# Performance work log

Hardware: AMD Instinct MI355X
Metric: run time of the kernel (lower is better)

## Reference

```python
import jax, jax.numpy as jnp
import numpy as np

BITW = 1
BITA = 3
BATCH = 8192
IN_CH = 4096
N_UNITS = 4096


def _quantize(x, k):
    # DoReFa uniform quantizer with straight-through estimator (round -> identity grad)
    n = float(2 ** k - 1)
    return x + jax.lax.stop_gradient(jnp.round(x * n) / n - x)


def _cabs(x):
    # clip magnitude to [0, 1]
    return jnp.minimum(1.0, jnp.abs(x))


def quantize_active(x, bitA):
    if bitA == 32:
        return x
    return _quantize(x, bitA)


def quantize_weight(w, bitW):
    if bitW == 32:
        return w
    if bitW == 1:
        # binary weights scaled by mean |w| (E is treated as constant)
        E = jax.lax.stop_gradient(jnp.mean(jnp.abs(w)))
        y = w / E
        # sign with straight-through gradient
        return (y + jax.lax.stop_gradient(jnp.sign(y) - y)) * E
    t = jnp.tanh(w)
    t = t / jnp.max(jnp.abs(t)) * 0.5 + 0.5
    return 2.0 * _quantize(t, bitW) - 1.0


def setup_inputs() -> dict:
    key = jax.random.key(0)
    k1, k2 = jax.random.split(key)
    inputs = jax.random.normal(k1, (BATCH, IN_CH), dtype=jnp.float32)
    # truncated_normal(stddev=0.1) init approximated with normal * 0.1
    W = jax.random.normal(k2, (IN_CH, N_UNITS), dtype=jnp.float32) * 0.1
    b = jnp.zeros((N_UNITS,), dtype=jnp.float32)
    return {"inputs": inputs, "W": W, "b": b}


def reference(inputs, W, b):
    q_in = quantize_active(_cabs(inputs), BITA)   # [B, IN] in {0..1} grid of 2^bitA-1 levels
    q_W = quantize_weight(W, BITW)                # [IN, OUT] binary (+-E)
    out = jnp.matmul(q_in, q_W) + b               # [B, OUT]
    return out
```

## Files before the change

kernel.cpp:

```cpp
#include <hip/hip_runtime.h>


static constexpr int BATCH  = 8192;
static constexpr int IN_CH  = 4096;
static constexpr int NUNITS = 4096;
static constexpr int TPB    = 256;

typedef int v4i __attribute__((ext_vector_type(4)));

static constexpr size_t A8_OFF   = 0;
static constexpr size_t A8_BYTES = (size_t)BATCH * IN_CH;
static constexpr size_t BT_OFF   = A8_OFF + A8_BYTES;
static constexpr size_t BT_BYTES = (size_t)NUNITS * IN_CH;
static constexpr int    NPART    = 4096;
static constexpr size_t PART_OFF = BT_OFF + BT_BYTES;
static constexpr size_t SCALE_OFF= PART_OFF + NPART * sizeof(float);

__global__ __launch_bounds__(TPB) void k_scale(const float* __restrict__ partials,
                                               float* __restrict__ scale) {
    __shared__ float red[TPB];
    float s = 0.f;
    for (int i = threadIdx.x; i < NPART; i += TPB) s += partials[i];
    red[threadIdx.x] = s;
    __syncthreads();
    for (int off = TPB / 2; off > 0; off >>= 1) {
        if ((int)threadIdx.x < off) red[threadIdx.x] += red[threadIdx.x + off];
        __syncthreads();
    }
    if (threadIdx.x == 0) {
        float E = red[0] / (float)((size_t)IN_CH * NUNITS);
        *scale = E / 7.0f;
    }
}

__device__ __forceinline__ unsigned int q4(float4 v) {
    unsigned int b0 = (unsigned int)(int)rintf(fminf(1.0f, fabsf(v.x)) * 7.0f);
    unsigned int b1 = (unsigned int)(int)rintf(fminf(1.0f, fabsf(v.y)) * 7.0f);
    unsigned int b2 = (unsigned int)(int)rintf(fminf(1.0f, fabsf(v.z)) * 7.0f);
    unsigned int b3 = (unsigned int)(int)rintf(fminf(1.0f, fabsf(v.w)) * 7.0f);
    return b0 | (b1 << 8) | (b2 << 16) | (b3 << 24);
}

__global__ __launch_bounds__(TPB) void k_quant_a(const float4* __restrict__ x4,
                                                 uint4* __restrict__ a16) {
    const size_t t = (size_t)blockIdx.x * TPB + threadIdx.x;
    uint4 o;
    o.x = q4(x4[t * 4 + 0]);
    o.y = q4(x4[t * 4 + 1]);
    o.z = q4(x4[t * 4 + 2]);
    o.w = q4(x4[t * 4 + 3]);
    a16[t] = o;
}

__global__ __launch_bounds__(TPB) void k_signT(const float* __restrict__ W,
                                               char* __restrict__ bt,
                                               float* __restrict__ partials) {
    __shared__ char tile[64][68];
    __shared__ float red[TPB];
    const int bk = blockIdx.x & 63;
    const int bn = blockIdx.x >> 6;
    const int t  = threadIdx.x;
    const int c  = t & 63;
    const int r0 = t >> 6;
    float asum = 0.f;
#pragma unroll
    for (int i = 0; i < 16; ++i) {
        int r = i * 4 + r0;
        float w = W[(size_t)(bk * 64 + r) * NUNITS + bn * 64 + c];
        asum += fabsf(w);
        tile[c][r] = (w > 0.f) ? 1 : ((w < 0.f) ? -1 : 0);
    }
    __syncthreads();
    const int n  = t >> 2;
    const int kk = (t & 3) * 16;
    char o[16];
#pragma unroll
    for (int j = 0; j < 16; ++j) o[j] = tile[n][kk + j];
    *(uint4*)(bt + (size_t)(bn * 64 + n) * IN_CH + bk * 64 + kk) = *(const uint4*)o;

    red[t] = asum;
    __syncthreads();
    for (int off = TPB / 2; off > 0; off >>= 1) {
        if (t < off) red[t] += red[t + off];
        __syncthreads();
    }
    if (t == 0) partials[blockIdx.x] = red[0];
}

__device__ __forceinline__ void gload_lds16(const void* g, void* l) {
    __builtin_amdgcn_global_load_lds((const __attribute__((address_space(1))) void*)g,
                                     (__attribute__((address_space(3))) void*)l,
                                     16, 0, 0);
}

#define VMCNT4   asm volatile("s_waitcnt vmcnt(4)" ::: "memory")
#define VMCNT0   asm volatile("s_waitcnt vmcnt(0)" ::: "memory")
#define LGKM0    asm volatile("s_waitcnt lgkmcnt(0)" ::: "memory")
#define BARRIER  __builtin_amdgcn_s_barrier()
#define PRIO1    __builtin_amdgcn_s_setprio(1)
#define PRIO0    __builtin_amdgcn_s_setprio(0)

static constexpr int NT = IN_CH / 128;

__global__ __launch_bounds__(512, 2) void k_gemm(const char* __restrict__ A8,
                                                 const char* __restrict__ BT,
                                                 const float* __restrict__ scale_p,
                                                 const float* __restrict__ bias,
                                                 float* __restrict__ out) {
    __shared__ char As[2][32768];
    __shared__ char Bs[2][32768];

    const int t    = threadIdx.x;
    const int bid  = blockIdx.x;
    const int swzb = (bid & 7) * 64 + (bid >> 3);
    const int bRow = swzb >> 4;
    const int bCol = swzb & 15;
    const int lane = t & 63;
    const int wid  = t >> 6;
    const int wm   = wid >> 2;
    const int wn   = wid & 3;
    const int lr   = lane & 15;
    const int lk4  = lane >> 4;

    const size_t aBase = (size_t)(bRow * 256) * IN_CH;
    const size_t bBase = (size_t)(bCol * 256) * IN_CH;

    const int ceff0 = (lk4 * 16) ^ ((lr & 7) << 4);
    const int ceff1 = ceff0 ^ 64;

    const int srow  = t >> 3;
    const int scol  = ((t & 7) * 16) ^ ((srow & 7) << 4);
    const int sldso = t * 16;

    v4i acc[8][4] = {};
    v4i a0[4][2], a1[4][2], b01[2][2], b23[2][2];

#define STAGE(kt, q)                                                                  \
    do {                                                                              \
        const int _b = (kt) & 1;                                                      \
        if ((q) < 4)                                                                  \
            gload_lds16(A8 + aBase + (size_t)((q) * 64 + srow) * IN_CH + (kt) * 128 + scol, \
                        &As[_b][(q & 3) * 8192 + sldso]);                             \
        else                                                                          \
            gload_lds16(BT + bBase + (size_t)(((q) - 4) * 64 + srow) * IN_CH + (kt) * 128 + scol, \
                        &Bs[_b][((q) - 4) * 8192 + sldso]);                           \
    } while (0)

#define READ_A0(Ab)                                                    \
    _Pragma("unroll") for (int m = 0; m < 4; ++m) {                    \
        const int ra = (wm * 128 + m * 16 + lr) * 128;                 \
        a0[m][0] = *(const v4i*)((Ab) + ra + ceff0);                   \
        a0[m][1] = *(const v4i*)((Ab) + ra + ceff1);                   \
    }
#define READ_A1(Ab)                                                    \
    _Pragma("unroll") for (int m = 0; m < 4; ++m) {                    \
        const int ra = (wm * 128 + (m + 4) * 16 + lr) * 128;           \
        a1[m][0] = *(const v4i*)((Ab) + ra + ceff0);                   \
        a1[m][1] = *(const v4i*)((Ab) + ra + ceff1);                   \
    }
#define READ_B01(Bb)                                                   \
    _Pragma("unroll") for (int n = 0; n < 2; ++n) {                    \
        const int rb = (wn * 64 + n * 16 + lr) * 128;                  \
        b01[n][0] = *(const v4i*)((Bb) + rb + ceff0);                  \
        b01[n][1] = *(const v4i*)((Bb) + rb + ceff1);                  \
    }
#define READ_B23(Bb)                                                   \
    _Pragma("unroll") for (int n = 0; n < 2; ++n) {                    \
        const int rb = (wn * 64 + (n + 2) * 16 + lr) * 128;            \
        b23[n][0] = *(const v4i*)((Bb) + rb + ceff0);                  \
        b23[n][1] = *(const v4i*)((Bb) + rb + ceff1);                  \
    }
#define MFMA16(arr, brr, mo, no)                                                       \
    PRIO1;                                                                             \
    _Pragma("unroll") for (int m = 0; m < 4; ++m)                                      \
        _Pragma("unroll") for (int n = 0; n < 2; ++n)                                  \
            _Pragma("unroll") for (int s = 0; s < 2; ++s)                              \
                acc[(mo) + m][(no) + n] = __builtin_amdgcn_mfma_i32_16x16x64_i8(       \
                    arr[m][s], brr[n][s], acc[(mo) + m][(no) + n], 0, 0, 0);           \
    PRIO0

#pragma unroll
    for (int q = 0; q < 8; ++q) STAGE(0, q);
    STAGE(1, 0); STAGE(1, 1); STAGE(1, 2); STAGE(1, 3);
    VMCNT4;
    BARRIER;

    for (int T = 0; T < NT; ++T) {
        const char* Ab = As[T & 1];
        const char* Bb = Bs[T & 1];

        READ_A0(Ab); READ_B01(Bb);
        if (T + 1 < NT) { STAGE(T + 1, 4); STAGE(T + 1, 5); STAGE(T + 1, 6); STAGE(T + 1, 7); }
        BARRIER; LGKM0;
        MFMA16(a0, b01, 0, 0);
        BARRIER;

        READ_B23(Bb);
        BARRIER; LGKM0;
        MFMA16(a0, b23, 0, 2);
        BARRIER;

        READ_A1(Ab);
        BARRIER; LGKM0;
        MFMA16(a1, b01, 4, 0);
        BARRIER;

        if (T + 2 < NT) { STAGE(T + 2, 0); STAGE(T + 2, 1); STAGE(T + 2, 2); STAGE(T + 2, 3); }
        if (T + 1 < NT) { VMCNT4; } else { VMCNT0; }
        BARRIER;
        MFMA16(a1, b23, 4, 2);
        BARRIER;
    }

    const float scale = *scale_p;
    const int orow0 = bRow * 256 + wm * 128;
    const int ocol0 = bCol * 256 + wn * 64;
#pragma unroll
    for (int m = 0; m < 8; ++m) {
#pragma unroll
        for (int n = 0; n < 4; ++n) {
            const int col = ocol0 + n * 16 + lr;
            const float bb = bias[col];
            const int rbase = orow0 + m * 16 + lk4 * 4;
#pragma unroll
            for (int j = 0; j < 4; ++j)
                out[(size_t)(rbase + j) * NUNITS + col] = scale * (float)acc[m][n][j] + bb;
        }
    }
#undef STAGE
#undef READ_A0
#undef READ_A1
#undef READ_B01
#undef READ_B23
#undef MFMA16
}

extern "C" void kernel_launch(void* const* d_in, const int* in_sizes, int n_in,
                              void* d_out, int out_size, void* d_ws, size_t ws_size,
                              hipStream_t stream) {
    const float* x  = (const float*)d_in[0];
    const float* W  = (const float*)d_in[1];
    const float* b  = (const float*)d_in[2];
    float* out      = (float*)d_out;

    char*  ws       = (char*)d_ws;
    char*  A8       = ws + A8_OFF;
    char*  BT       = ws + BT_OFF;
    float* partials = (float*)(ws + PART_OFF);
    float* scale    = (float*)(ws + SCALE_OFF);

    k_signT<<<(IN_CH / 64) * (NUNITS / 64), TPB, 0, stream>>>(W, BT, partials);
    k_scale<<<1, TPB, 0, stream>>>(partials, scale);
    k_quant_a<<<(BATCH * (IN_CH / 16)) / TPB, TPB, 0, stream>>>((const float4*)x, (uint4*)A8);
    k_gemm<<<(BATCH / 256) * (NUNITS / 256), 512, 0, stream>>>(A8, BT, scale, b, out);
}
```

Measured before the change: 196.2 us.

## Unroll GEMM main loop by two and interleave stage loads finer across MFMA phases

The K-loop is unrolled by two with fixed LDS buffer pointers, and the global-to-LDS staging of each tile is split into pairs of loads placed in every MFMA phase. The wait becomes vmcnt(6), so more loads stay in flight. The aim is a steadier memory stream and fewer stalls at the phase boundaries. The risk is a wrong ordering between staged quarters and LDS reads if the quarter-to-phase mapping does not match the data each phase consumes.

```diff
diff --git a/kernel.cpp b/kernel.cpp
--- a/kernel.cpp
+++ b/kernel.cpp
@@ -93,7 +93,7 @@
                                      16, 0, 0);
 }
 
-#define VMCNT4   asm volatile("s_waitcnt vmcnt(4)" ::: "memory")
+#define VMCNT6   asm volatile("s_waitcnt vmcnt(6)" ::: "memory")
 #define VMCNT0   asm volatile("s_waitcnt vmcnt(0)" ::: "memory")
 #define LGKM0    asm volatile("s_waitcnt lgkmcnt(0)" ::: "memory")
 #define BARRIER  __builtin_amdgcn_s_barrier()
@@ -179,38 +179,88 @@
                     arr[m][s], brr[n][s], acc[(mo) + m][(no) + n], 0, 0, 0);           \
     PRIO0
 
-#pragma unroll
-    for (int q = 0; q < 8; ++q) STAGE(0, q);
-    STAGE(1, 0); STAGE(1, 1); STAGE(1, 2); STAGE(1, 3);
-    VMCNT4;
-    BARRIER;
-
-    for (int T = 0; T < NT; ++T) {
-        const char* Ab = As[T & 1];
-        const char* Bb = Bs[T & 1];
-
-        READ_A0(Ab); READ_B01(Bb);
-        if (T + 1 < NT) { STAGE(T + 1, 4); STAGE(T + 1, 5); STAGE(T + 1, 6); STAGE(T + 1, 7); }
+    STAGE(0, 0); STAGE(0, 1); STAGE(0, 2); STAGE(0, 3);
+    STAGE(0, 4); STAGE(0, 5); STAGE(0, 6); STAGE(0, 7);
+    STAGE(1, 0); STAGE(1, 2); STAGE(1, 4); STAGE(1, 5); STAGE(1, 6); STAGE(1, 7);
+    VMCNT6;
+    BARRIER;
+
+    const char* Ab0 = As[0]; const char* Bb0 = Bs[0];
+    const char* Ab1 = As[1]; const char* Bb1 = Bs[1];
+
+    for (int i = 0; i < 15; ++i) {
+        const int T = 2 * i;
+        READ_A0(Ab0); READ_B01(Bb0);
+        STAGE(T + 1, 1); STAGE(T + 1, 3);
         BARRIER; LGKM0;
         MFMA16(a0, b01, 0, 0);
         BARRIER;
-
-        READ_B23(Bb);
+        READ_B23(Bb0);
+        STAGE(T + 2, 0); STAGE(T + 2, 2);
         BARRIER; LGKM0;
         MFMA16(a0, b23, 0, 2);
         BARRIER;
-
-        READ_A1(Ab);
+        READ_A1(Ab0);
+        STAGE(T + 2, 4); STAGE(T + 2, 5);
         BARRIER; LGKM0;
         MFMA16(a1, b01, 4, 0);
         BARRIER;
-
-        if (T + 2 < NT) { STAGE(T + 2, 0); STAGE(T + 2, 1); STAGE(T + 2, 2); STAGE(T + 2, 3); }
-        if (T + 1 < NT) { VMCNT4; } else { VMCNT0; }
+        STAGE(T + 2, 6); STAGE(T + 2, 7);
+        VMCNT6;
         BARRIER;
         MFMA16(a1, b23, 4, 2);
         BARRIER;
-    }
+        READ_A0(Ab1); READ_B01(Bb1);
+        STAGE(T + 2, 1); STAGE(T + 2, 3);
+        BARRIER; LGKM0;
+        MFMA16(a0, b01, 0, 0);
+        BARRIER;
+        READ_B23(Bb1);
+        STAGE(T + 3, 0); STAGE(T + 3, 2);
+        BARRIER; LGKM0;
+        MFMA16(a0, b23, 0, 2);
+        BARRIER;
+        READ_A1(Ab1);
+        STAGE(T + 3, 4); STAGE(T + 3, 5);
+        BARRIER; LGKM0;
+        MFMA16(a1, b01, 4, 0);
+        BARRIER;
+        STAGE(T + 3, 6); STAGE(T + 3, 7);
+        VMCNT6;
+        BARRIER;
+        MFMA16(a1, b23, 4, 2);
+        BARRIER;
+    }
+
+    READ_A0(Ab0); READ_B01(Bb0);
+    STAGE(31, 1); STAGE(31, 3);
+    BARRIER; LGKM0;
+    MFMA16(a0, b01, 0, 0);
+    BARRIER;
+    READ_B23(Bb0);
+    BARRIER; LGKM0;
+    MFMA16(a0, b23, 0, 2);
+    BARRIER;
+    READ_A1(Ab0);
+    BARRIER; LGKM0;
+    MFMA16(a1, b01, 4, 0);
+    BARRIER;
+    VMCNT0;
+    BARRIER;
+    MFMA16(a1, b23, 4, 2);
+    BARRIER;
+    READ_A0(Ab1); READ_B01(Bb1);
+    BARRIER; LGKM0;
+    MFMA16(a0, b01, 0, 0);
+    BARRIER;
+    READ_B23(Bb1);
+    BARRIER; LGKM0;
+    MFMA16(a0, b23, 0, 2);
+    BARRIER;
+    READ_A1(Ab1);
+    BARRIER; LGKM0;
+    MFMA16(a1, b01, 4, 0);
+    MFMA16(a1, b23, 4, 2);
 
     const float scale = *scale_p;
     const int orow0 = bRow * 256 + wm * 128;
```

After: 199.9 us. Within noise of the previous version (+1.9%).
